# Optimization experiments

Measured on AMD Instinct MI355X. Metric: run time of the kernel, lower is better.

Reference implementation:

```python
import jax, jax.numpy as jnp
import numpy as np

EMBED_DIM = 1024
NUM_HEADS = 16
HEAD_DIM = EMBED_DIM // NUM_HEADS
SCALING = HEAD_DIM ** -0.5


def setup_inputs() -> dict:
    key = jax.random.key(0)
    ks = jax.random.split(key, 10)
    B, T, D = 4, 2048, EMBED_DIM
    s = 0.02
    return {
        "hidden_states": jax.random.normal(ks[0], (B, T, D), jnp.float32),
        "attention_mask": jnp.zeros((B, 1, T, T), jnp.float32),
        "Wq": jax.random.normal(ks[1], (D, D), jnp.float32) * s,
        "bq": jnp.zeros((D,), jnp.float32),
        "Wk": jax.random.normal(ks[2], (D, D), jnp.float32) * s,
        "bk": jnp.zeros((D,), jnp.float32),
        "Wv": jax.random.normal(ks[3], (D, D), jnp.float32) * s,
        "bv": jnp.zeros((D,), jnp.float32),
        "Wo": jax.random.normal(ks[4], (D, D), jnp.float32) * s,
        "bo": jnp.zeros((D,), jnp.float32),
    }


def reference(hidden_states, attention_mask, Wq, bq, Wk, bk, Wv, bv, Wo, bo):
    B, T, D = hidden_states.shape
    H, Hd = NUM_HEADS, HEAD_DIM
    # projections (torch Linear: x @ W.T + b; here W stored as (D_in, D_out))
    q = (hidden_states @ Wq + bq) * SCALING
    k = hidden_states @ Wk + bk
    v = hidden_states @ Wv + bv
    q = q.reshape(B, T, H, Hd).transpose(0, 2, 1, 3)  # [B,H,T,Hd]
    k = k.reshape(B, T, H, Hd).transpose(0, 2, 1, 3)
    v = v.reshape(B, T, H, Hd).transpose(0, 2, 1, 3)
    # eager attention: full [B,H,T,T] scores + additive mask + softmax
    scores = jnp.einsum("bhtd,bhsd->bhts", q, k)
    scores = scores + attention_mask[:, :, :, : k.shape[2]]
    attn_weights = jax.nn.softmax(scores, axis=-1)
    attn_output = jnp.einsum("bhts,bhsd->bhtd", attn_weights, v)
    attn_output = attn_output.transpose(0, 2, 1, 3).reshape(B, T, D)
    attn_output = attn_output @ Wo + bo
    return attn_output
```

## Files before the change

kernel.cpp:

```cpp
#include <hip/hip_runtime.h>
#include <hip/hip_bf16.h>
#include <cstdint>

#define TT 2048
#define DD 1024
#define NH 16
#define HD 64
#define NB 4
#define SCALING 0.125f
#define LOG2E 1.44269504088896340736f

typedef __bf16 bf16;
typedef __attribute__((ext_vector_type(8))) __bf16 bf16x8;
typedef __attribute__((ext_vector_type(4))) __bf16 bf16x4;
typedef __attribute__((ext_vector_type(4))) float f32x4;

__device__ __forceinline__ void gload_lds16(const bf16* g, bf16* l) {
    __builtin_amdgcn_global_load_lds(
        (__attribute__((address_space(1))) const void*)g,
        (__attribute__((address_space(3))) void*)l, 16, 0, 0);
}


__global__ void k_convert_x(const float* __restrict__ x, bf16* __restrict__ xb) {
    size_t i = ((size_t)blockIdx.x * 256 + threadIdx.x) * 4;
    float4 v = *(const float4*)(x + i);
    bf16x4 o;
    o[0] = (bf16)v.x; o[1] = (bf16)v.y; o[2] = (bf16)v.z; o[3] = (bf16)v.w;
    *(bf16x4*)(xb + i) = o;
}

__global__ void k_transpose_w(const float* __restrict__ Wq, const float* __restrict__ Wk,
                              const float* __restrict__ Wv, const float* __restrict__ Wo,
                              bf16* __restrict__ Wt) {
    __shared__ float tile[32][33];
    int mat = blockIdx.z;
    const float* w = mat == 0 ? Wq : (mat == 1 ? Wk : (mat == 2 ? Wv : Wo));
    int n0 = blockIdx.x * 32, k0 = blockIdx.y * 32;
    int tx = threadIdx.x, ty = threadIdx.y;
    tile[ty][tx] = w[(size_t)(k0 + ty) * DD + n0 + tx];
    __syncthreads();
    Wt[(size_t)mat * DD * DD + (size_t)(n0 + ty) * DD + k0 + tx] = (bf16)tile[tx][ty];
}

__global__ void k_mask_flags(const float* __restrict__ mask, int* __restrict__ flags) {
    int bb = blockIdx.z, t0 = blockIdx.y * 128, s0 = blockIdx.x * 64;
    const float* mp = mask + ((size_t)bb * TT + t0) * TT + s0;
    int c = (threadIdx.x & 15) * 4;
    int r0 = threadIdx.x >> 4;
    int any = 0;
    for (int r = r0; r < 128; r += 16) {
        float4 v = *(const float4*)(mp + (size_t)r * TT + c);
        any |= (v.x != 0.f) | (v.y != 0.f) | (v.z != 0.f) | (v.w != 0.f);
    }
    any = __any(any) ? 1 : 0;
    __shared__ int s_any[4];
    if ((threadIdx.x & 63) == 0) s_any[threadIdx.x >> 6] = any;
    __syncthreads();
    if (threadIdx.x == 0)
        flags[(bb * 16 + blockIdx.y) * 32 + blockIdx.x] = s_any[0] | s_any[1] | s_any[2] | s_any[3];
}

__device__ __forceinline__ void gemm128_main(const bf16* __restrict__ A, const bf16* __restrict__ Bt,
                                             int m0, int n0, int K,
                                             bf16* As, bf16* Bs, f32x4 acc[4][4]) {
    const int tid = threadIdx.x;
    const int w = tid >> 6, lane = tid & 63;
    const int wr = w >> 1, wc = w & 1, quad = lane >> 4, l16 = lane & 15;
    f32x4 zero = {0.f, 0.f, 0.f, 0.f};
#pragma unroll
    for (int mi = 0; mi < 4; mi++)
#pragma unroll
        for (int ni = 0; ni < 4; ni++) acc[mi][ni] = zero;

    for (int k0 = 0; k0 < K; k0 += 32) {
        if (k0) __syncthreads();
#pragma unroll
        for (int j = 0; j < 2; j++) {
            int idx = w * 128 + j * 64 + lane;
            int row = idx >> 2, kc = (idx & 3) * 8;
            gload_lds16(A + (size_t)(m0 + row) * K + k0 + kc, As + idx * 8);
            gload_lds16(Bt + (size_t)(n0 + row) * K + k0 + kc, Bs + idx * 8);
        }
        __syncthreads();
        bf16x8 af[4], bfv[4];
#pragma unroll
        for (int i = 0; i < 4; i++)
            af[i] = *(const bf16x8*)(As + (wr * 64 + i * 16 + l16) * 32 + quad * 8);
#pragma unroll
        for (int i = 0; i < 4; i++)
            bfv[i] = *(const bf16x8*)(Bs + (wc * 64 + i * 16 + l16) * 32 + quad * 8);
#pragma unroll
        for (int mi = 0; mi < 4; mi++)
#pragma unroll
            for (int ni = 0; ni < 4; ni++)
                acc[mi][ni] = __builtin_amdgcn_mfma_f32_16x16x32_bf16(af[mi], bfv[ni], acc[mi][ni], 0, 0, 0);
    }
}

__global__ __launch_bounds__(256) void k_gemm_qkv(const bf16* __restrict__ Xb, const bf16* __restrict__ Wt,
                                                  const float* __restrict__ bq, const float* __restrict__ bk,
                                                  const float* __restrict__ bv,
                                                  bf16* __restrict__ qb, bf16* __restrict__ kb,
                                                  bf16* __restrict__ vt) {
    __shared__ bf16 As[128 * 32];
    __shared__ bf16 Bs[128 * 32];
    int m0 = blockIdx.y * 128, n0 = blockIdx.x * 128;
    f32x4 acc[4][4];
    gemm128_main(Xb, Wt, m0, n0, DD, As, Bs, acc);

    const int tid = threadIdx.x, w = tid >> 6, lane = tid & 63;
    const int wr = w >> 1, wc = w & 1, quad = lane >> 4, l16 = lane & 15;
    int which = n0 >> 10;
    const float* bias = which == 0 ? bq : (which == 1 ? bk : bv);
#pragma unroll
    for (int mi = 0; mi < 4; mi++)
#pragma unroll
        for (int ni = 0; ni < 4; ni++) {
            int gn = n0 + wc * 64 + ni * 16 + l16;
            int nn = gn & 1023, h = nn >> 6, d = nn & 63;
            float bb_ = bias[nn];
#pragma unroll
            for (int r = 0; r < 4; r++) {
                int gm = m0 + wr * 64 + mi * 16 + quad * 4 + r;
                int bb = gm >> 11, t = gm & 2047;
                float v = acc[mi][ni][r] + bb_;
                if (which == 0)
                    qb[(((size_t)bb * NH + h) * TT + t) * HD + d] = (bf16)(v * SCALING);
                else if (which == 1)
                    kb[(((size_t)bb * NH + h) * TT + t) * HD + d] = (bf16)v;
                else
                    vt[(((size_t)bb * NH + h) * HD + d) * TT + t] = (bf16)v;
            }
        }
}

__global__ __launch_bounds__(256) void k_attn(const bf16* __restrict__ qb, const bf16* __restrict__ kb,
                                              const bf16* __restrict__ vt, const float* __restrict__ mask,
                                              const int* __restrict__ flags, bf16* __restrict__ ob) {
    __shared__ bf16 Qs[128 * 64];
    __shared__ bf16 Ks[64 * 64];
    __shared__ bf16 Vs[64 * 64];
    __shared__ bf16 Ps[128 * 64];

    const int tq0 = blockIdx.x * 128;
    const int h = blockIdx.y;
    const int bb = blockIdx.z;
    const int tid = threadIdx.x, w = tid >> 6, lane = tid & 63;
    const int quad = lane >> 4, l16 = lane & 15;

    const bf16* Qg = qb + (((size_t)bb * NH + h) * TT + tq0) * HD;
    const bf16* Kg = kb + ((size_t)bb * NH + h) * TT * HD;
    const bf16* Vg = vt + ((size_t)bb * NH + h) * HD * TT;

#pragma unroll
    for (int j = 0; j < 4; j++) {
        int idx = (w * 4 + j) * 64 + lane;
        int row = idx >> 3, cs = idx & 7;
        int c = cs ^ (row & 7);
        gload_lds16(Qg + (size_t)row * HD + c * 8, Qs + idx * 8);
    }

    bf16x8 ones;
#pragma unroll
    for (int i = 0; i < 8; i++) ones[i] = (bf16)1.0f;

    f32x4 oa[2][4];
    f32x4 lacc[2];
    f32x4 zero = {0.f, 0.f, 0.f, 0.f};
#pragma unroll
    for (int mi = 0; mi < 2; mi++) {
        lacc[mi] = zero;
#pragma unroll
        for (int ni = 0; ni < 4; ni++) oa[mi][ni] = zero;
    }

    const int fbase = (bb * 16 + blockIdx.x) * 32;

    for (int s0 = 0; s0 < TT; s0 += 64) {
        __syncthreads();
#pragma unroll
        for (int j = 0; j < 2; j++) {
            int idx = (w * 2 + j) * 64 + lane;
            int row = idx >> 3, cs = idx & 7;
            int c = cs ^ (row & 7);
            gload_lds16(Kg + (size_t)(s0 + row) * HD + c * 8, Ks + idx * 8);
            gload_lds16(Vg + (size_t)row * TT + s0 + c * 8, Vs + idx * 8);
        }
        __syncthreads();

        f32x4 sa[2][4];
#pragma unroll
        for (int mi = 0; mi < 2; mi++)
#pragma unroll
            for (int ni = 0; ni < 4; ni++) sa[mi][ni] = zero;
#pragma unroll
        for (int kk = 0; kk < 2; kk++) {
            const int csw = ((kk * 4 + quad) ^ (l16 & 7)) * 8;
            bf16x8 aq[2], bk8[4];
#pragma unroll
            for (int mi = 0; mi < 2; mi++)
                aq[mi] = *(const bf16x8*)(Qs + (w * 32 + mi * 16 + l16) * 64 + csw);
#pragma unroll
            for (int ni = 0; ni < 4; ni++)
                bk8[ni] = *(const bf16x8*)(Ks + (ni * 16 + l16) * 64 + csw);
#pragma unroll
            for (int mi = 0; mi < 2; mi++)
#pragma unroll
                for (int ni = 0; ni < 4; ni++)
                    sa[mi][ni] = __builtin_amdgcn_mfma_f32_16x16x32_bf16(aq[mi], bk8[ni], sa[mi][ni], 0, 0, 0);
        }

        if (flags[fbase + (s0 >> 6)]) {
            const float* mp = mask + ((size_t)bb * TT + tq0) * TT + s0;
#pragma unroll
            for (int mi = 0; mi < 2; mi++)
#pragma unroll
                for (int ni = 0; ni < 4; ni++)
#pragma unroll
                    for (int r = 0; r < 4; r++)
                        sa[mi][ni][r] += mp[(size_t)(w * 32 + mi * 16 + quad * 4 + r) * TT + ni * 16 + l16];
        }

#pragma unroll
        for (int mi = 0; mi < 2; mi++)
#pragma unroll
            for (int r = 0; r < 4; r++) {
                int row = w * 32 + mi * 16 + quad * 4 + r;
                int rsw = (quad * 4 + r) & 7;
#pragma unroll
                for (int ni = 0; ni < 4; ni++) {
                    float p = exp2f(sa[mi][ni][r] * LOG2E);
                    int col = ni * 16 + l16;
                    Ps[row * 64 + ((col >> 3) ^ rsw) * 8 + (col & 7)] = (bf16)p;
                }
            }

#pragma unroll
        for (int kk = 0; kk < 2; kk++) {
            const int csw = ((kk * 4 + quad) ^ (l16 & 7)) * 8;
            bf16x8 ap[2], bv8[4];
#pragma unroll
            for (int mi = 0; mi < 2; mi++)
                ap[mi] = *(const bf16x8*)(Ps + (w * 32 + mi * 16 + l16) * 64 + csw);
#pragma unroll
            for (int ni = 0; ni < 4; ni++)
                bv8[ni] = *(const bf16x8*)(Vs + (ni * 16 + l16) * 64 + csw);
#pragma unroll
            for (int mi = 0; mi < 2; mi++)
                lacc[mi] = __builtin_amdgcn_mfma_f32_16x16x32_bf16(ap[mi], ones, lacc[mi], 0, 0, 0);
#pragma unroll
            for (int mi = 0; mi < 2; mi++)
#pragma unroll
                for (int ni = 0; ni < 4; ni++)
                    oa[mi][ni] = __builtin_amdgcn_mfma_f32_16x16x32_bf16(ap[mi], bv8[ni], oa[mi][ni], 0, 0, 0);
        }
    }

#pragma unroll
    for (int mi = 0; mi < 2; mi++)
#pragma unroll
        for (int r = 0; r < 4; r++) {
            float inv = 1.f / lacc[mi][r];
            int trow = tq0 + w * 32 + mi * 16 + quad * 4 + r;
#pragma unroll
            for (int ni = 0; ni < 4; ni++) {
                float v = oa[mi][ni][r] * inv;
                ob[((size_t)bb * TT + trow) * DD + h * HD + ni * 16 + l16] = (bf16)v;
            }
        }
}

__global__ __launch_bounds__(256) void k_gemm_out(const bf16* __restrict__ Ob, const bf16* __restrict__ Wot,
                                                  const float* __restrict__ bo, float* __restrict__ out) {
    __shared__ bf16 As[128 * 32];
    __shared__ bf16 Bs[128 * 32];
    int m0 = blockIdx.y * 128, n0 = blockIdx.x * 128;
    f32x4 acc[4][4];
    gemm128_main(Ob, Wot, m0, n0, DD, As, Bs, acc);

    const int tid = threadIdx.x, w = tid >> 6, lane = tid & 63;
    const int wr = w >> 1, wc = w & 1, quad = lane >> 4, l16 = lane & 15;
#pragma unroll
    for (int mi = 0; mi < 4; mi++)
#pragma unroll
        for (int ni = 0; ni < 4; ni++) {
            int gn = n0 + wc * 64 + ni * 16 + l16;
            float bb_ = bo[gn];
#pragma unroll
            for (int r = 0; r < 4; r++) {
                int gm = m0 + wr * 64 + mi * 16 + quad * 4 + r;
                out[(size_t)gm * DD + gn] = acc[mi][ni][r] + bb_;
            }
        }
}

extern "C" void kernel_launch(void* const* d_in, const int* in_sizes, int n_in,
                              void* d_out, int out_size, void* d_ws, size_t ws_size,
                              hipStream_t stream) {
    const float* hidden = (const float*)d_in[0];
    const float* mask   = (const float*)d_in[1];
    const float* Wq     = (const float*)d_in[2];
    const float* bq     = (const float*)d_in[3];
    const float* Wk     = (const float*)d_in[4];
    const float* bk     = (const float*)d_in[5];
    const float* Wv     = (const float*)d_in[6];
    const float* bv     = (const float*)d_in[7];
    const float* Wo     = (const float*)d_in[8];
    const float* bo     = (const float*)d_in[9];
    float* out = (float*)d_out;
    char* ws = (char*)d_ws;

    const size_t MB = 1024 * 1024;
    bf16* Xb   = (bf16*)(ws);
    bf16* Wt   = (bf16*)(ws + 16 * MB);
    bf16* qb   = (bf16*)(ws + 24 * MB);
    bf16* kb   = (bf16*)(ws + 40 * MB);
    bf16* vt   = (bf16*)(ws + 56 * MB);
    bf16* ob   = (bf16*)(ws + 72 * MB);
    int* flags = (int*)(ws + 88 * MB);

    hipLaunchKernelGGL(k_convert_x, dim3(8192), dim3(256), 0, stream, hidden, Xb);
    hipLaunchKernelGGL(k_transpose_w, dim3(32, 32, 4), dim3(32, 32), 0, stream, Wq, Wk, Wv, Wo, Wt);
    hipLaunchKernelGGL(k_mask_flags, dim3(32, 16, 4), dim3(256), 0, stream, mask, flags);
    hipLaunchKernelGGL(k_gemm_qkv, dim3(24, 64), dim3(256), 0, stream, Xb, Wt, bq, bk, bv, qb, kb, vt);
    hipLaunchKernelGGL(k_attn, dim3(16, 16, 4), dim3(256), 0, stream, qb, kb, vt, mask, flags, ob);
    hipLaunchKernelGGL(k_gemm_out, dim3(8, 64), dim3(256), 0, stream, ob, Wt + (size_t)3 * DD * DD, bo, out);
}
```

Before: 423.6 us.

## Fuse prep kernels, keep P in registers, and stage V transpose via LDS

Merges x conversion and weight transpose into one launch, and folds the mask-flag scan into the QKV GEMM grid by interleaving flag blocks with GEMM tiles. The attention kernel now computes S transposed (K as A operand), so exp(P) values land in registers in the layout needed for the PV MFMA, removing the Ps shared-memory round trip. The log2e factor is folded into the Q scale, and V is stored transposed through an LDS staging buffer for coalesced writes, with a new swizzle for V tiles. These changes cut launches, LDS traffic and uncoalesced stores, but add more complex indexing and branch divergence between block roles.

```diff
diff --git a/kernel.cpp b/kernel.cpp
--- a/kernel.cpp
+++ b/kernel.cpp
@@ -9,6 +9,7 @@
 #define NB 4
 #define SCALING 0.125f
 #define LOG2E 1.44269504088896340736f
+#define QSCALE (0.125f * 1.44269504088896340736f)
 
 typedef __bf16 bf16;
 typedef __attribute__((ext_vector_type(8))) __bf16 bf16x8;
@@ -21,44 +22,32 @@
         (__attribute__((address_space(3))) void*)l, 16, 0, 0);
 }
 
-
-__global__ void k_convert_x(const float* __restrict__ x, bf16* __restrict__ xb) {
-    size_t i = ((size_t)blockIdx.x * 256 + threadIdx.x) * 4;
-    float4 v = *(const float4*)(x + i);
-    bf16x4 o;
-    o[0] = (bf16)v.x; o[1] = (bf16)v.y; o[2] = (bf16)v.z; o[3] = (bf16)v.w;
-    *(bf16x4*)(xb + i) = o;
-}
-
-__global__ void k_transpose_w(const float* __restrict__ Wq, const float* __restrict__ Wk,
-                              const float* __restrict__ Wv, const float* __restrict__ Wo,
-                              bf16* __restrict__ Wt) {
-    __shared__ float tile[32][33];
-    int mat = blockIdx.z;
+__global__ __launch_bounds__(256) void k_prep(const float* __restrict__ x, bf16* __restrict__ xb,
+                                              const float* __restrict__ Wq, const float* __restrict__ Wk,
+                                              const float* __restrict__ Wv, const float* __restrict__ Wo,
+                                              bf16* __restrict__ Wt) {
+    __shared__ float tile_s[32][33];
+    int bid = blockIdx.x, tid = threadIdx.x;
+    if (bid < 8192) {
+        size_t i = ((size_t)bid * 256 + tid) * 4;
+        float4 v = *(const float4*)(x + i);
+        bf16x4 o;
+        o[0] = (bf16)v.x; o[1] = (bf16)v.y; o[2] = (bf16)v.z; o[3] = (bf16)v.w;
+        *(bf16x4*)(xb + i) = o;
+        return;
+    }
+    int b2 = bid - 8192;
+    int mat = b2 >> 10, tl = b2 & 1023;
+    int n0 = (tl & 31) * 32, k0 = (tl >> 5) * 32;
     const float* w = mat == 0 ? Wq : (mat == 1 ? Wk : (mat == 2 ? Wv : Wo));
-    int n0 = blockIdx.x * 32, k0 = blockIdx.y * 32;
-    int tx = threadIdx.x, ty = threadIdx.y;
-    tile[ty][tx] = w[(size_t)(k0 + ty) * DD + n0 + tx];
+    int tx = tid & 31, ty = tid >> 5;
+#pragma unroll
+    for (int i = 0; i < 4; i++)
+        tile_s[ty + 8 * i][tx] = w[(size_t)(k0 + ty + 8 * i) * DD + n0 + tx];
     __syncthreads();
-    Wt[(size_t)mat * DD * DD + (size_t)(n0 + ty) * DD + k0 + tx] = (bf16)tile[tx][ty];
-}
-
-__global__ void k_mask_flags(const float* __restrict__ mask, int* __restrict__ flags) {
-    int bb = blockIdx.z, t0 = blockIdx.y * 128, s0 = blockIdx.x * 64;
-    const float* mp = mask + ((size_t)bb * TT + t0) * TT + s0;
-    int c = (threadIdx.x & 15) * 4;
-    int r0 = threadIdx.x >> 4;
-    int any = 0;
-    for (int r = r0; r < 128; r += 16) {
-        float4 v = *(const float4*)(mp + (size_t)r * TT + c);
-        any |= (v.x != 0.f) | (v.y != 0.f) | (v.z != 0.f) | (v.w != 0.f);
-    }
-    any = __any(any) ? 1 : 0;
-    __shared__ int s_any[4];
-    if ((threadIdx.x & 63) == 0) s_any[threadIdx.x >> 6] = any;
-    __syncthreads();
-    if (threadIdx.x == 0)
-        flags[(bb * 16 + blockIdx.y) * 32 + blockIdx.x] = s_any[0] | s_any[1] | s_any[2] | s_any[3];
+#pragma unroll
+    for (int i = 0; i < 4; i++)
+        Wt[(size_t)mat * DD * DD + (size_t)(n0 + ty + 8 * i) * DD + k0 + tx] = (bf16)tile_s[tx][ty + 8 * i];
 }
 
 __device__ __forceinline__ void gemm128_main(const bf16* __restrict__ A, const bf16* __restrict__ Bt,
@@ -102,37 +91,94 @@
                                                   const float* __restrict__ bq, const float* __restrict__ bk,
                                                   const float* __restrict__ bv,
                                                   bf16* __restrict__ qb, bf16* __restrict__ kb,
-                                                  bf16* __restrict__ vt) {
-    __shared__ bf16 As[128 * 32];
-    __shared__ bf16 Bs[128 * 32];
-    int m0 = blockIdx.y * 128, n0 = blockIdx.x * 128;
+                                                  bf16* __restrict__ vt,
+                                                  const float* __restrict__ mask, int* __restrict__ flags) {
+    __shared__ bf16 smem[8448];
+    __shared__ int s_any[4];
+    const int bid = blockIdx.x, tid = threadIdx.x;
+    const int grp = bid / 7, rem = bid % 7;
+
+    if (rem >= 3) {
+        int fid = grp * 4 + (rem - 3);
+        int st = fid & 31, tt = (fid >> 5) & 15, bbm = fid >> 9;
+        const float* mp = mask + ((size_t)bbm * TT + tt * 128) * TT + st * 64;
+        int c = (tid & 15) * 4;
+        int r0 = tid >> 4;
+        int any = 0;
+        for (int r = r0; r < 128; r += 16) {
+            float4 v = *(const float4*)(mp + (size_t)r * TT + c);
+            any |= (v.x != 0.f) | (v.y != 0.f) | (v.z != 0.f) | (v.w != 0.f);
+        }
+        any = __any(any) ? 1 : 0;
+        if ((tid & 63) == 0) s_any[tid >> 6] = any;
+        __syncthreads();
+        if (tid == 0)
+            flags[(bbm * 16 + tt) * 32 + st] = s_any[0] | s_any[1] | s_any[2] | s_any[3];
+        return;
+    }
+
+    int g = grp * 3 + rem;
+    int bx = g % 24, by = g / 24;
+    int m0 = by * 128, n0 = bx * 128;
+    bf16* As = smem;
+    bf16* Bs = smem + 4096;
     f32x4 acc[4][4];
     gemm128_main(Xb, Wt, m0, n0, DD, As, Bs, acc);
 
-    const int tid = threadIdx.x, w = tid >> 6, lane = tid & 63;
+    const int w = tid >> 6, lane = tid & 63;
     const int wr = w >> 1, wc = w & 1, quad = lane >> 4, l16 = lane & 15;
-    int which = n0 >> 10;
-    const float* bias = which == 0 ? bq : (which == 1 ? bk : bv);
-#pragma unroll
-    for (int mi = 0; mi < 4; mi++)
-#pragma unroll
-        for (int ni = 0; ni < 4; ni++) {
-            int gn = n0 + wc * 64 + ni * 16 + l16;
-            int nn = gn & 1023, h = nn >> 6, d = nn & 63;
-            float bb_ = bias[nn];
-#pragma unroll
-            for (int r = 0; r < 4; r++) {
-                int gm = m0 + wr * 64 + mi * 16 + quad * 4 + r;
-                int bb = gm >> 11, t = gm & 2047;
-                float v = acc[mi][ni][r] + bb_;
-                if (which == 0)
-                    qb[(((size_t)bb * NH + h) * TT + t) * HD + d] = (bf16)(v * SCALING);
-                else if (which == 1)
-                    kb[(((size_t)bb * NH + h) * TT + t) * HD + d] = (bf16)v;
-                else
-                    vt[(((size_t)bb * NH + h) * HD + d) * TT + t] = (bf16)v;
-            }
-        }
+    const int which = n0 >> 10;
+    const int bbk = m0 >> 11, tbase = m0 & 2047;
+
+    if (which < 2) {
+        const float* bias = which == 0 ? bq : bk;
+#pragma unroll
+        for (int mi = 0; mi < 4; mi++)
+#pragma unroll
+            for (int ni = 0; ni < 4; ni++) {
+                int nn = (n0 & 1023) + wc * 64 + ni * 16 + l16;
+                int h = nn >> 6, d = nn & 63;
+                float bb_ = bias[nn];
+#pragma unroll
+                for (int r = 0; r < 4; r++) {
+                    int t = tbase + wr * 64 + mi * 16 + quad * 4 + r;
+                    float v = acc[mi][ni][r] + bb_;
+                    if (which == 0)
+                        qb[(((size_t)bbk * NH + h) * TT + t) * HD + d] = (bf16)(v * QSCALE);
+                    else
+                        kb[(((size_t)bbk * NH + h) * TT + t) * HD + d] = (bf16)v;
+                }
+            }
+    } else {
+        const int nn0 = n0 & 1023;
+#pragma unroll
+        for (int phase = 0; phase < 2; phase++) {
+            __syncthreads();
+            if (wc == phase) {
+#pragma unroll
+                for (int mi = 0; mi < 4; mi++)
+#pragma unroll
+                    for (int ni = 0; ni < 4; ni++) {
+                        int nn_l = ni * 16 + l16;
+                        float bb_ = bv[nn0 + phase * 64 + nn_l];
+#pragma unroll
+                        for (int r = 0; r < 4; r++) {
+                            int t_l = wr * 64 + mi * 16 + quad * 4 + r;
+                            smem[nn_l * 132 + t_l] = (bf16)(acc[mi][ni][r] + bb_);
+                        }
+                    }
+            }
+            __syncthreads();
+            int hh = (nn0 + phase * 64) >> 6;
+#pragma unroll
+            for (int i = 0; i < 4; i++) {
+                int idx = i * 256 + tid;
+                int rr = idx >> 4, cc = (idx & 15) * 8;
+                bf16x8 vv = *(const bf16x8*)(smem + rr * 132 + cc);
+                *(bf16x8*)(vt + (((size_t)bbk * NH + hh) * HD + rr) * TT + tbase + cc) = vv;
+            }
+        }
+    }
 }
 
 __global__ __launch_bounds__(256) void k_attn(const bf16* __restrict__ qb, const bf16* __restrict__ kb,
@@ -141,11 +187,9 @@
     __shared__ bf16 Qs[128 * 64];
     __shared__ bf16 Ks[64 * 64];
     __shared__ bf16 Vs[64 * 64];
-    __shared__ bf16 Ps[128 * 64];
 
     const int tq0 = blockIdx.x * 128;
-    const int h = blockIdx.y;
-    const int bb = blockIdx.z;
+    const int h = blockIdx.y, bb = blockIdx.z;
     const int tid = threadIdx.x, w = tid >> 6, lane = tid & 63;
     const int quad = lane >> 4, l16 = lane & 15;
 
@@ -157,8 +201,7 @@
     for (int j = 0; j < 4; j++) {
         int idx = (w * 4 + j) * 64 + lane;
         int row = idx >> 3, cs = idx & 7;
-        int c = cs ^ (row & 7);
-        gload_lds16(Qg + (size_t)row * HD + c * 8, Qs + idx * 8);
+        gload_lds16(Qg + (size_t)row * HD + (cs ^ (row & 7)) * 8, Qs + idx * 8);
     }
 
     bf16x8 ones;
@@ -169,103 +212,107 @@
     f32x4 lacc[2];
     f32x4 zero = {0.f, 0.f, 0.f, 0.f};
 #pragma unroll
-    for (int mi = 0; mi < 2; mi++) {
-        lacc[mi] = zero;
-#pragma unroll
-        for (int ni = 0; ni < 4; ni++) oa[mi][ni] = zero;
+    for (int qi = 0; qi < 2; qi++) {
+        lacc[qi] = zero;
+#pragma unroll
+        for (int ni = 0; ni < 4; ni++) oa[qi][ni] = zero;
     }
 
     const int fbase = (bb * 16 + blockIdx.x) * 32;
+    const int vkey = l16 & 14;
 
     for (int s0 = 0; s0 < TT; s0 += 64) {
         __syncthreads();
 #pragma unroll
         for (int j = 0; j < 2; j++) {
             int idx = (w * 2 + j) * 64 + lane;
-            int row = idx >> 3, cs = idx & 7;
-            int c = cs ^ (row & 7);
-            gload_lds16(Kg + (size_t)(s0 + row) * HD + c * 8, Ks + idx * 8);
-            gload_lds16(Vg + (size_t)row * TT + s0 + c * 8, Vs + idx * 8);
+            int row = idx >> 3, m = idx & 7;
+            gload_lds16(Kg + (size_t)(s0 + row) * HD + (m ^ (row & 7)) * 8, Ks + idx * 8);
+            gload_lds16(Vg + (size_t)row * TT + s0 + ((2 * m) ^ (row & 14)) * 4, Vs + idx * 8);
         }
         __syncthreads();
 
-        f32x4 sa[2][4];
-#pragma unroll
-        for (int mi = 0; mi < 2; mi++)
-#pragma unroll
-            for (int ni = 0; ni < 4; ni++) sa[mi][ni] = zero;
-#pragma unroll
-        for (int kk = 0; kk < 2; kk++) {
-            const int csw = ((kk * 4 + quad) ^ (l16 & 7)) * 8;
-            bf16x8 aq[2], bk8[4];
-#pragma unroll
-            for (int mi = 0; mi < 2; mi++)
-                aq[mi] = *(const bf16x8*)(Qs + (w * 32 + mi * 16 + l16) * 64 + csw);
-#pragma unroll
-            for (int ni = 0; ni < 4; ni++)
-                bk8[ni] = *(const bf16x8*)(Ks + (ni * 16 + l16) * 64 + csw);
-#pragma unroll
-            for (int mi = 0; mi < 2; mi++)
-#pragma unroll
-                for (int ni = 0; ni < 4; ni++)
-                    sa[mi][ni] = __builtin_amdgcn_mfma_f32_16x16x32_bf16(aq[mi], bk8[ni], sa[mi][ni], 0, 0, 0);
+        f32x4 st[4][2];
+#pragma unroll
+        for (int si = 0; si < 4; si++)
+#pragma unroll
+            for (int qi = 0; qi < 2; qi++) st[si][qi] = zero;
+#pragma unroll
+        for (int kd = 0; kd < 2; kd++) {
+            const int csw = ((kd * 4 + quad) ^ (l16 & 7)) * 8;
+            bf16x8 kf[4], qf[2];
+#pragma unroll
+            for (int si = 0; si < 4; si++)
+                kf[si] = *(const bf16x8*)(Ks + (si * 16 + l16) * 64 + csw);
+#pragma unroll
+            for (int qi = 0; qi < 2; qi++)
+                qf[qi] = *(const bf16x8*)(Qs + (w * 32 + qi * 16 + l16) * 64 + csw);
+#pragma unroll
+            for (int si = 0; si < 4; si++)
+#pragma unroll
+                for (int qi = 0; qi < 2; qi++)
+                    st[si][qi] = __builtin_amdgcn_mfma_f32_16x16x32_bf16(kf[si], qf[qi], st[si][qi], 0, 0, 0);
         }
 
         if (flags[fbase + (s0 >> 6)]) {
             const float* mp = mask + ((size_t)bb * TT + tq0) * TT + s0;
 #pragma unroll
-            for (int mi = 0; mi < 2; mi++)
+            for (int si = 0; si < 4; si++)
+#pragma unroll
+                for (int qi = 0; qi < 2; qi++)
+#pragma unroll
+                    for (int r = 0; r < 4; r++)
+                        st[si][qi][r] += mp[(size_t)(w * 32 + qi * 16 + l16) * TT + si * 16 + quad * 4 + r] * LOG2E;
+        }
+
+        bf16 ep[4][2][4];
+#pragma unroll
+        for (int si = 0; si < 4; si++)
+#pragma unroll
+            for (int qi = 0; qi < 2; qi++)
+#pragma unroll
+                for (int r = 0; r < 4; r++)
+                    ep[si][qi][r] = (bf16)exp2f(st[si][qi][r]);
+
+#pragma unroll
+        for (int kk = 0; kk < 2; kk++) {
+            bf16x8 ap[2];
+#pragma unroll
+            for (int qi = 0; qi < 2; qi++)
+#pragma unroll
+                for (int j = 0; j < 8; j++)
+                    ap[qi][j] = ep[2 * kk + (j >> 2)][qi][j & 3];
+            bf16x8 bv8[4];
+#pragma unroll
+            for (int ni = 0; ni < 4; ni++) {
+                const int rbase = (ni * 16 + l16) * 64;
+                const int c0 = ((kk * 8 + quad) ^ vkey) * 4;
+                const int c1 = ((kk * 8 + quad + 4) ^ vkey) * 4;
+                bf16x4 lo = *(const bf16x4*)(Vs + rbase + c0);
+                bf16x4 hi = *(const bf16x4*)(Vs + rbase + c1);
+#pragma unroll
+                for (int e = 0; e < 4; e++) { bv8[ni][e] = lo[e]; bv8[ni][e + 4] = hi[e]; }
+            }
+#pragma unroll
+            for (int qi = 0; qi < 2; qi++)
+                lacc[qi] = __builtin_amdgcn_mfma_f32_16x16x32_bf16(ap[qi], ones, lacc[qi], 0, 0, 0);
+#pragma unroll
+            for (int qi = 0; qi < 2; qi++)
 #pragma unroll
                 for (int ni = 0; ni < 4; ni++)
-#pragma unroll
-                    for (int r = 0; r < 4; r++)
-                        sa[mi][ni][r] += mp[(size_t)(w * 32 + mi * 16 + quad * 4 + r) * TT + ni * 16 + l16];
-        }
-
-#pragma unroll
-        for (int mi = 0; mi < 2; mi++)
-#pragma unroll
-            for (int r = 0; r < 4; r++) {
-                int row = w * 32 + mi * 16 + quad * 4 + r;
-                int rsw = (quad * 4 + r) & 7;
-#pragma unroll
-                for (int ni = 0; ni < 4; ni++) {
-                    float p = exp2f(sa[mi][ni][r] * LOG2E);
-                    int col = ni * 16 + l16;
-                    Ps[row * 64 + ((col >> 3) ^ rsw) * 8 + (col & 7)] = (bf16)p;
-                }
-            }
-
-#pragma unroll
-        for (int kk = 0; kk < 2; kk++) {
-            const int csw = ((kk * 4 + quad) ^ (l16 & 7)) * 8;
-            bf16x8 ap[2], bv8[4];
-#pragma unroll
-            for (int mi = 0; mi < 2; mi++)
-                ap[mi] = *(const bf16x8*)(Ps + (w * 32 + mi * 16 + l16) * 64 + csw);
-#pragma unroll
-            for (int ni = 0; ni < 4; ni++)
-                bv8[ni] = *(const bf16x8*)(Vs + (ni * 16 + l16) * 64 + csw);
-#pragma unroll
-            for (int mi = 0; mi < 2; mi++)
-                lacc[mi] = __builtin_amdgcn_mfma_f32_16x16x32_bf16(ap[mi], ones, lacc[mi], 0, 0, 0);
-#pragma unroll
-            for (int mi = 0; mi < 2; mi++)
-#pragma unroll
-                for (int ni = 0; ni < 4; ni++)
-                    oa[mi][ni] = __builtin_amdgcn_mfma_f32_16x16x32_bf16(ap[mi], bv8[ni], oa[mi][ni], 0, 0, 0);
-        }
-    }
-
-#pragma unroll
-    for (int mi = 0; mi < 2; mi++)
+                    oa[qi][ni] = __builtin_amdgcn_mfma_f32_16x16x32_bf16(ap[qi], bv8[ni], oa[qi][ni], 0, 0, 0);
+        }
+    }
+
+#pragma unroll
+    for (int qi = 0; qi < 2; qi++)
 #pragma unroll
         for (int r = 0; r < 4; r++) {
-            float inv = 1.f / lacc[mi][r];
-            int trow = tq0 + w * 32 + mi * 16 + quad * 4 + r;
+            float inv = 1.f / lacc[qi][r];
+            int trow = tq0 + w * 32 + qi * 16 + quad * 4 + r;
 #pragma unroll
             for (int ni = 0; ni < 4; ni++) {
-                float v = oa[mi][ni][r] * inv;
+                float v = oa[qi][ni][r] * inv;
                 ob[((size_t)bb * TT + trow) * DD + h * HD + ni * 16 + l16] = (bf16)v;
             }
         }
@@ -320,10 +367,8 @@
     bf16* ob   = (bf16*)(ws + 72 * MB);
     int* flags = (int*)(ws + 88 * MB);
 
-    hipLaunchKernelGGL(k_convert_x, dim3(8192), dim3(256), 0, stream, hidden, Xb);
-    hipLaunchKernelGGL(k_transpose_w, dim3(32, 32, 4), dim3(32, 32), 0, stream, Wq, Wk, Wv, Wo, Wt);
-    hipLaunchKernelGGL(k_mask_flags, dim3(32, 16, 4), dim3(256), 0, stream, mask, flags);
-    hipLaunchKernelGGL(k_gemm_qkv, dim3(24, 64), dim3(256), 0, stream, Xb, Wt, bq, bk, bv, qb, kb, vt);
+    hipLaunchKernelGGL(k_prep, dim3(12288), dim3(256), 0, stream, hidden, Xb, Wq, Wk, Wv, Wo, Wt);
+    hipLaunchKernelGGL(k_gemm_qkv, dim3(3584), dim3(256), 0, stream, Xb, Wt, bq, bk, bv, qb, kb, vt, mask, flags);
     hipLaunchKernelGGL(k_attn, dim3(16, 16, 4), dim3(256), 0, stream, qb, kb, vt, mask, flags, ob);
     hipLaunchKernelGGL(k_gemm_out, dim3(8, 64), dim3(256), 0, stream, ob, Wt + (size_t)3 * DD * DD, bo, out);
 }
```

Measured after the change: 404.7 us. 4.5% less time.
